# Optimization experiments

Measured on AMD Instinct MI355X. Metric: run time of the kernel, lower is better.

## Reference

```python
import jax, jax.numpy as jnp
import numpy as np

BN_EPS = 1e-5


def setup_inputs() -> dict:
    key = jax.random.key(0)
    ks = jax.random.split(key, 6)
    P, D_IN, H, N_NODES = 2_000_000, 3, 128, 20_000
    x = jax.random.normal(ks[0], (P, D_IN), dtype=jnp.float32)
    batch_idx = jax.random.randint(ks[1], (P,), 0, N_NODES, dtype=jnp.int64)
    W1 = jax.random.normal(ks[2], (D_IN, H), dtype=jnp.float32) * 0.5
    b1 = jax.random.normal(ks[3], (H,), dtype=jnp.float32) * 0.1
    gamma = jnp.ones((H,), dtype=jnp.float32)
    beta = jnp.zeros((H,), dtype=jnp.float32)
    running_mean = jnp.zeros((H,), dtype=jnp.float32)
    running_var = jnp.ones((H,), dtype=jnp.float32)
    W2 = jax.random.normal(ks[4], (H, H), dtype=jnp.float32) * (1.0 / np.sqrt(H))
    b2 = jax.random.normal(ks[5], (H,), dtype=jnp.float32) * 0.1
    return {"x": x, "batch_idx": batch_idx, "num_nodes": N_NODES,
            "W1": W1, "b1": b1, "gamma": gamma, "beta": beta,
            "running_mean": running_mean, "running_var": running_var,
            "W2": W2, "b2": b2}


def reference(x, batch_idx, num_nodes, W1, b1, gamma, beta,
              running_mean, running_var, W2, b2):
    # per-point MLP: Linear -> BatchNorm1d (eval: running stats) -> ReLU -> Linear -> ReLU
    h = x @ W1 + b1                                        # [P, H]
    h = (h - running_mean) * jax.lax.rsqrt(running_var + BN_EPS) * gamma + beta
    h = jax.nn.relu(h)
    h = jax.nn.relu(h @ W2 + b2)                            # [P, H], values >= 0
    # scatter_max by node; torch_scatter fills empty segments with 0,
    # and since h >= 0 post-ReLU, clamping the -inf fill to 0 is exact.
    node_feats = jax.ops.segment_max(h, batch_idx, num_segments=num_nodes)
    return jnp.maximum(node_feats, 0.0)                     # [num_nodes, H]
```

## Files before the change

### kernel.cpp

```cpp
#include <hip/hip_runtime.h>
#include <hip/hip_bf16.h>

#define H 128
#define TILE_PTS 32
#define ROW_STRIDE 136
#define NBLK 512
#define BT 1024
#define BSH 3
#define NPB (1 << BSH)
#define CAP 1024
#define RAWN (CAP + 32)
#define HBUF (TILE_PTS * ROW_STRIDE)

typedef __attribute__((ext_vector_type(8))) short short8;
typedef __attribute__((ext_vector_type(4))) float float4v;
typedef __attribute__((ext_vector_type(2))) float float2v;
typedef __attribute__((ext_vector_type(4))) int int4v;
typedef _Float16 half8 __attribute__((ext_vector_type(8)));
typedef _Float16 half2 __attribute__((ext_vector_type(2)));

static __device__ __forceinline__ unsigned short f2bf(float f) {
    unsigned u = __float_as_uint(f);
    unsigned r = (u + 0x7fffu + ((u >> 16) & 1u)) >> 16;
    return (unsigned short)r;
}
static __device__ __forceinline__ unsigned pkbf(float a, float b) {
    __hip_bfloat162 h = __float22bfloat162_rn(float2{a, b});
    return *reinterpret_cast<unsigned*>(&h);
}
static __device__ __forceinline__ unsigned short f2h(float f) {
    _Float16 h = (_Float16)f;
    unsigned short u;
    __builtin_memcpy(&u, &h, 2);
    return u;
}
static __device__ __forceinline__ float h2f(unsigned short us) {
    _Float16 h;
    __builtin_memcpy(&h, &us, 2);
    return (float)h;
}

__global__ __launch_bounds__(BT)
void scatter_slot(const int* __restrict__ bidx, const float* __restrict__ x,
                  const float* __restrict__ W2, unsigned short* __restrict__ W2T,
                  int* __restrict__ gcnt, uint2* __restrict__ xb,
                  int P, int nbuk) {
    extern __shared__ int lh[];
    const int b = blockIdx.x, t = threadIdx.x;
    for (int i = b * BT + t; i < H * H; i += NBLK * BT) {
        int n = i >> 7, k = i & 127;
        W2T[i] = f2h(W2[k * H + n]);
    }
    for (int i = t; i < nbuk; i += BT) lh[i] = 0;
    __syncthreads();
    const int chunk4 = (((P + NBLK - 1) / NBLK) + 3) & ~3;
    const int lo = b * chunk4;
    const int hi = (lo + chunk4 < P) ? lo + chunk4 : P;
    for (int p4 = lo + 4 * t; p4 < hi; p4 += 4 * BT) {
        if (p4 + 4 <= hi) {
            int4v i4 = *(const int4v*)&bidx[p4];
            atomicAdd(&lh[i4.x >> BSH], 1);
            atomicAdd(&lh[i4.y >> BSH], 1);
            atomicAdd(&lh[i4.z >> BSH], 1);
            atomicAdd(&lh[i4.w >> BSH], 1);
        } else {
            for (int p = p4; p < hi; ++p) atomicAdd(&lh[bidx[p] >> BSH], 1);
        }
    }
    __syncthreads();
    for (int i = t; i < nbuk; i += BT) {
        int c = lh[i];
        lh[i] = (c > 0) ? atomicAdd(&gcnt[i], c) : 0;
    }
    __syncthreads();
    auto emit = [&](int idx, float x0, float x1, float x2) {
        int pos = atomicAdd(&lh[idx >> BSH], 1);
        if (pos < CAP) {
            uint2 r;
            r.x = (unsigned)f2h(x0) | ((unsigned)f2h(x1) << 16);
            r.y = (unsigned)f2h(x2) | ((unsigned)(idx & (NPB - 1)) << 16);
            xb[(size_t)(idx >> BSH) * CAP + pos] = r;
        }
    };
    for (int p4 = lo + 4 * t; p4 < hi; p4 += 4 * BT) {
        if (p4 + 4 <= hi) {
            int4v i4 = *(const int4v*)&bidx[p4];
            float4v xa = *(const float4v*)(x + (size_t)p4 * 3);
            float4v xbv = *(const float4v*)(x + (size_t)p4 * 3 + 4);
            float4v xc = *(const float4v*)(x + (size_t)p4 * 3 + 8);
            emit(i4.x, xa[0], xa[1], xa[2]);
            emit(i4.y, xa[3], xbv[0], xbv[1]);
            emit(i4.z, xbv[2], xbv[3], xc[0]);
            emit(i4.w, xc[1], xc[2], xc[3]);
        } else {
            for (int p = p4; p < hi; ++p)
                emit(bidx[p], x[p * 3 + 0], x[p * 3 + 1], x[p * 3 + 2]);
        }
    }
}

__global__ __launch_bounds__(256, 4)
void node_kernel18(const uint2* __restrict__ xb, const int* __restrict__ gcnt,
                   const float* __restrict__ W1, const float* __restrict__ b1,
                   const float* __restrict__ gamma, const float* __restrict__ beta,
                   const float* __restrict__ rmean, const float* __restrict__ rvar,
                   const unsigned short* __restrict__ W2T, const float* __restrict__ b2,
                   float* __restrict__ out, int N)
{
    __shared__ __align__(16) unsigned short pool[2 * HBUF];
    __shared__ __align__(16) uint2 srt[RAWN];
    __shared__ int basec[NPB + 1];
    __shared__ int curw[4][NPB];

    const int bk   = blockIdx.x;
    const int t    = threadIdx.x;
    const int lane = t & 63;
    const int wave = t >> 6;
    const int g  = t & 15;
    const int q  = t >> 4;
    const int c0 = g * 8;

    half2 w1h[3][4], b1h[4];
    #pragma unroll
    for (int jp = 0; jp < 4; ++jp) {
        #pragma unroll
        for (int e = 0; e < 2; ++e) {
            int c = c0 + 2 * jp + e;
            float sc = gamma[c] * rsqrtf(rvar[c] + 1e-5f);
            w1h[0][jp][e] = (_Float16)(W1[0 * H + c] * sc);
            w1h[1][jp][e] = (_Float16)(W1[1 * H + c] * sc);
            w1h[2][jp][e] = (_Float16)(W1[2 * H + c] * sc);
            b1h[jp][e]    = (_Float16)((b1[c] - rmean[c]) * sc + beta[c]);
        }
    }

    const int bn = lane & 15;
    const int kq = (lane >> 4) * 8;
    half8 bfrag[2][4];
    float  b2v[2];
    #pragma unroll
    for (int nt = 0; nt < 2; ++nt) {
        const int nn = wave * 32 + nt * 16 + bn;
        b2v[nt] = b2[nn];
        #pragma unroll
        for (int kk = 0; kk < 4; ++kk)
            bfrag[nt][kk] = *(const half8*)(const void*)&W2T[nn * H + kk * 32 + kq];
    }

    uint2* raw = (uint2*)pool;
    int n_b = gcnt[bk];
    if (n_b > CAP) n_b = CAP;
    const uint2* src = xb + (size_t)bk * CAP;
    for (int p = t; p < n_b; p += 256) raw[p] = src[p];
    if (t < 4 * NPB) ((int*)curw)[t] = 0;
    __syncthreads();
    for (int p = t; p < n_b; p += 256)
        atomicAdd(&curw[wave][raw[p].y >> 16], 1);
    __syncthreads();
    if (t == 0) {
        int run = 0;
        #pragma unroll
        for (int i = 0; i < NPB; ++i) {
            basec[i] = run;
            #pragma unroll
            for (int w = 0; w < 4; ++w) {
                int c = curw[w][i]; curw[w][i] = run; run += c;
            }
        }
        basec[NPB] = run;
    }
    __syncthreads();
    for (int p = t; p < n_b; p += 256) {
        uint2 r = raw[p];
        int pos = atomicAdd(&curw[wave][r.y >> 16], 1);
        srt[pos] = r;
    }
    for (int p = n_b + t; p < n_b + TILE_PTS; p += 256)
        if (p < RAWN) srt[p] = uint2{0u, 0u};
    __syncthreads();

    const float4v zero4 = {0.f, 0.f, 0.f, 0.f};
    const float NEG_INF = -__builtin_inff();
    const half2 zero2h = {(_Float16)0.f, (_Float16)0.f};
    const int nodebase = bk << BSH;
    const int nlocal = (N - nodebase < NPB) ? (N - nodebase) : NPB;

    const int st0 = q * ROW_STRIDE + c0;
    const int st1 = (q + 16) * ROW_STRIDE + c0;
    const int ar  = bn * ROW_STRIDE + kq;

    #define STAGE_PT(r, hs, so)                                            \
    {                                                                      \
        half2 a0 = __builtin_bit_cast(half2,                               \
            __builtin_amdgcn_perm(0u, (r).x, 0x01000100u));                \
        half2 a1 = __builtin_bit_cast(half2,                               \
            __builtin_amdgcn_perm(0u, (r).x, 0x03020302u));                \
        half2 a2 = __builtin_bit_cast(half2,                               \
            __builtin_amdgcn_perm(0u, (r).y, 0x01000100u));                \
        int4v pk;                                                          \
        _Pragma("unroll")                                                  \
        for (int jp = 0; jp < 4; ++jp) {                                   \
            half2 hh = b1h[jp];                                            \
            hh = __builtin_elementwise_fma(a0, w1h[0][jp], hh);            \
            hh = __builtin_elementwise_fma(a1, w1h[1][jp], hh);            \
            hh = __builtin_elementwise_fma(a2, w1h[2][jp], hh);            \
            hh = __builtin_elementwise_max(hh, zero2h);                    \
            pk[jp] = __builtin_bit_cast(int, hh);                          \
        }                                                                  \
        *(int4v*)(void*)&(hs)[so] = pk;                                    \
    }

    for (int j = 0; j < nlocal; ++j) {
        const int startj = basec[j];
        const int n      = basec[j + 1] - startj;
        const int ntiles = (n + TILE_PTS - 1) >> 5;

        float2v vm0 = {NEG_INF, NEG_INF};
        float2v vm1 = {NEG_INF, NEG_INF};

        if (ntiles > 0) {
            unsigned short* hb = pool;
            unsigned short* hs = pool + HBUF;
            {
                uint2 r0 = srt[startj + q];
                uint2 r1 = srt[startj + q + 16];
                STAGE_PT(r0, hb, st0);
                STAGE_PT(r1, hb, st1);
            }
            __syncthreads();

            for (int tile = 0; tile < ntiles; ++tile) {
                const int tb = tile * TILE_PTS;
                const bool have = (tile + 1 < ntiles);

                uint2 n0, n1;
                if (have) {
                    n0 = srt[startj + tb + TILE_PTS + q];
                    n1 = srt[startj + tb + TILE_PTS + 16 + q];
                }

                float4v acc00, acc01, acc10, acc11;
                {
                    half8 a0v = *(const half8*)(const void*)&hb[ar];
                    half8 a1v = *(const half8*)(const void*)&hb[ar + 16 * ROW_STRIDE];
                    acc00 = __builtin_amdgcn_mfma_f32_16x16x32_f16(a0v, bfrag[0][0], zero4, 0, 0, 0);
                    acc01 = __builtin_amdgcn_mfma_f32_16x16x32_f16(a0v, bfrag[1][0], zero4, 0, 0, 0);
                    acc10 = __builtin_amdgcn_mfma_f32_16x16x32_f16(a1v, bfrag[0][0], zero4, 0, 0, 0);
                    acc11 = __builtin_amdgcn_mfma_f32_16x16x32_f16(a1v, bfrag[1][0], zero4, 0, 0, 0);
                }
                #pragma unroll
                for (int kk = 1; kk < 4; ++kk) {
                    half8 a0v = *(const half8*)(const void*)&hb[ar + kk * 32];
                    half8 a1v = *(const half8*)(const void*)&hb[ar + 16 * ROW_STRIDE + kk * 32];
                    acc00 = __builtin_amdgcn_mfma_f32_16x16x32_f16(a0v, bfrag[0][kk], acc00, 0, 0, 0);
                    acc01 = __builtin_amdgcn_mfma_f32_16x16x32_f16(a0v, bfrag[1][kk], acc01, 0, 0, 0);
                    acc10 = __builtin_amdgcn_mfma_f32_16x16x32_f16(a1v, bfrag[0][kk], acc10, 0, 0, 0);
                    acc11 = __builtin_amdgcn_mfma_f32_16x16x32_f16(a1v, bfrag[1][kk], acc11, 0, 0, 0);
                }

                if (have) {
                    STAGE_PT(n0, hs, st0);
                    STAGE_PT(n1, hs, st1);
                }

                if (tb + TILE_PTS <= n) {
                    vm0 = __builtin_elementwise_max(vm0, float2v{acc00[0], acc00[1]});
                    vm0 = __builtin_elementwise_max(vm0, float2v{acc00[2], acc00[3]});
                    vm0 = __builtin_elementwise_max(vm0, float2v{acc10[0], acc10[1]});
                    vm0 = __builtin_elementwise_max(vm0, float2v{acc10[2], acc10[3]});
                    vm1 = __builtin_elementwise_max(vm1, float2v{acc01[0], acc01[1]});
                    vm1 = __builtin_elementwise_max(vm1, float2v{acc01[2], acc01[3]});
                    vm1 = __builtin_elementwise_max(vm1, float2v{acc11[0], acc11[1]});
                    vm1 = __builtin_elementwise_max(vm1, float2v{acc11[2], acc11[3]});
                } else {
                    const int r0base = (lane >> 4) * 4;
                    #pragma unroll
                    for (int r = 0; r < 4; ++r) {
                        const bool v0 = (tb + r0base + r) < n;
                        const bool v1 = (tb + 16 + r0base + r) < n;
                        vm0[r & 1] = fmaxf(vm0[r & 1], v0 ? acc00[r] : NEG_INF);
                        vm1[r & 1] = fmaxf(vm1[r & 1], v0 ? acc01[r] : NEG_INF);
                        vm0[r & 1] = fmaxf(vm0[r & 1], v1 ? acc10[r] : NEG_INF);
                        vm1[r & 1] = fmaxf(vm1[r & 1], v1 ? acc11[r] : NEG_INF);
                    }
                }
                __syncthreads();
                unsigned short* tmp = hb; hb = hs; hs = tmp;
            }
        }

        float vmax0 = fmaxf(vm0[0], vm0[1]);
        float vmax1 = fmaxf(vm1[0], vm1[1]);
        vmax0 = fmaxf(vmax0, __shfl_xor(vmax0, 16, 64));
        vmax0 = fmaxf(vmax0, __shfl_xor(vmax0, 32, 64));
        vmax1 = fmaxf(vmax1, __shfl_xor(vmax1, 16, 64));
        vmax1 = fmaxf(vmax1, __shfl_xor(vmax1, 32, 64));
        if (lane < 16) {
            float* orow = out + (size_t)(nodebase + j) * H + wave * 32;
            orow[lane]      = fmaxf(vmax0 + b2v[0], 0.f);
            orow[16 + lane] = fmaxf(vmax1 + b2v[1], 0.f);
        }
    }
    #undef STAGE_PT
}

__global__ void histB_kernel(const int* __restrict__ bidx, int* __restrict__ counts, int P) {
    int p = blockIdx.x * 256 + threadIdx.x;
    if (p < P) atomicAdd(&counts[bidx[p]], 1);
}
__global__ __launch_bounds__(1024)
void scanB_kernel(const int* __restrict__ counts, int* __restrict__ starts,
                  int* __restrict__ cursor, int N) {
    __shared__ int sums[1024];
    const int t = threadIdx.x;
    const int chunk = (N + 1023) >> 10;
    const int lo = t * chunk;
    const int hi = (lo + chunk < N) ? lo + chunk : N;
    int s = 0;
    for (int i = lo; i < hi; ++i) s += counts[i];
    sums[t] = s;
    __syncthreads();
    #pragma unroll
    for (int off = 1; off < 1024; off <<= 1) {
        int a = (t >= off) ? sums[t - off] : 0;
        __syncthreads();
        sums[t] += a;
        __syncthreads();
    }
    int run = sums[t] - s;
    for (int i = lo; i < hi; ++i) { starts[i] = run; cursor[i] = run; run += counts[i]; }
    if (t == 1023) starts[N] = sums[1023];
}
__global__ void scatterB_kernel(const int* __restrict__ bidx, const float* __restrict__ x,
                                int* __restrict__ cursor, uint2* __restrict__ xs, int P) {
    int p = blockIdx.x * 256 + threadIdx.x;
    if (p < P) {
        int pos = atomicAdd(&cursor[bidx[p]], 1);
        uint2 r;
        r.x = (unsigned)f2h(x[p * 3 + 0]) | ((unsigned)f2h(x[p * 3 + 1]) << 16);
        r.y = (unsigned)f2h(x[p * 3 + 2]);
        xs[pos] = r;
    }
}
__global__ void convw2_kernel(const float* __restrict__ W2, unsigned short* __restrict__ W2T) {
    int i = blockIdx.x * 256 + threadIdx.x;
    if (i < H * H) {
        int n = i >> 7, k = i & 127;
        W2T[i] = f2bf(W2[k * H + n]);
    }
}

__global__ __launch_bounds__(256, 4)
void node_kernelB(const uint2* __restrict__ xs,
                  const int*   __restrict__ starts,
                  const float* __restrict__ W1, const float* __restrict__ b1,
                  const float* __restrict__ gamma, const float* __restrict__ beta,
                  const float* __restrict__ rmean, const float* __restrict__ rvar,
                  const unsigned short* __restrict__ W2T, const float* __restrict__ b2,
                  float* __restrict__ out, int N)
{
    __shared__ __align__(16) unsigned short h1s[2][TILE_PTS * ROW_STRIDE];
    const int t = threadIdx.x, lane = t & 63, wave = t >> 6;
    const int g = t & 15, q = t >> 4, c0 = g * 8;
    float2v w1f2[3][4], b1f2[4];
    #pragma unroll
    for (int jp = 0; jp < 4; ++jp)
        #pragma unroll
        for (int e = 0; e < 2; ++e) {
            int c = c0 + 2 * jp + e;
            float sc = gamma[c] * rsqrtf(rvar[c] + 1e-5f);
            w1f2[0][jp][e] = W1[0 * H + c] * sc;
            w1f2[1][jp][e] = W1[1 * H + c] * sc;
            w1f2[2][jp][e] = W1[2 * H + c] * sc;
            b1f2[jp][e]    = (b1[c] - rmean[c]) * sc + beta[c];
        }
    const int bn = lane & 15, kq = (lane >> 4) * 8;
    short8 bfrag[2][4]; float b2v[2];
    #pragma unroll
    for (int nt = 0; nt < 2; ++nt) {
        const int nn = wave * 32 + nt * 16 + bn;
        b2v[nt] = b2[nn];
        #pragma unroll
        for (int kk = 0; kk < 4; ++kk)
            bfrag[nt][kk] = *(const short8*)&W2T[nn * H + kk * 32 + kq];
    }
    const float4v zero4 = {0.f, 0.f, 0.f, 0.f};
    const float NEG_INF = -__builtin_inff();
    const float2v zero2 = {0.f, 0.f};
    for (int node = blockIdx.x; node < N; node += gridDim.x) {
        const int start = starts[node];
        const int n = starts[node + 1] - start;
        const int ntiles = (n + TILE_PTS - 1) >> 5;
        float2v vmax2[2];
        vmax2[0] = float2v{NEG_INF, NEG_INF};
        vmax2[1] = float2v{NEG_INF, NEG_INF};
        auto loadx = [&](int tb, float xv[2][3]) {
            #pragma unroll
            for (int i = 0; i < 2; ++i) {
                uint2 r = xs[start + tb + q + 16 * i];
                xv[i][0] = h2f((unsigned short)(r.x & 0xffffu));
                xv[i][1] = h2f((unsigned short)(r.x >> 16));
                xv[i][2] = h2f((unsigned short)(r.y & 0xffffu));
            }
        };
        auto stage = [&](const float xv[2][3], unsigned short* buf) {
            #pragma unroll
            for (int i = 0; i < 2; ++i) {
                const int pl = q + 16 * i;
                float2v a0 = {xv[i][0], xv[i][0]};
                float2v a1 = {xv[i][1], xv[i][1]};
                float2v a2 = {xv[i][2], xv[i][2]};
                int4v pk;
                #pragma unroll
                for (int jp = 0; jp < 4; ++jp) {
                    float2v h = b1f2[jp];
                    h = __builtin_elementwise_fma(a0, w1f2[0][jp], h);
                    h = __builtin_elementwise_fma(a1, w1f2[1][jp], h);
                    h = __builtin_elementwise_fma(a2, w1f2[2][jp], h);
                    h = __builtin_elementwise_max(h, zero2);
                    pk[jp] = (int)pkbf(h[0], h[1]);
                }
                *(int4v*)(void*)&buf[pl * ROW_STRIDE + c0] = pk;
            }
        };
        if (ntiles > 0) {
            float xv[2][3];
            loadx(0, xv);
            stage(xv, h1s[0]);
            __syncthreads();
            int pb = 0;
            for (int tile = 0; tile < ntiles; ++tile) {
                const int tb = tile * TILE_PTS;
                const bool havenext = (tile + 1 < ntiles);
                float nx[2][3];
                if (havenext) loadx(tb + TILE_PTS, nx);
                float4v acc[2][2];
                const unsigned short* hb = h1s[pb];
                {
                    short8 a0 = *(const short8*)&hb[bn * ROW_STRIDE + kq];
                    short8 a1 = *(const short8*)&hb[(16 + bn) * ROW_STRIDE + kq];
                    #pragma unroll
                    for (int nt = 0; nt < 2; ++nt) {
                        acc[0][nt] = __builtin_amdgcn_mfma_f32_16x16x32_bf16(a0, bfrag[nt][0], zero4, 0, 0, 0);
                        acc[1][nt] = __builtin_amdgcn_mfma_f32_16x16x32_bf16(a1, bfrag[nt][0], zero4, 0, 0, 0);
                    }
                }
                #pragma unroll
                for (int kk = 1; kk < 4; ++kk) {
                    short8 a0 = *(const short8*)&hb[bn * ROW_STRIDE + kk * 32 + kq];
                    short8 a1 = *(const short8*)&hb[(16 + bn) * ROW_STRIDE + kk * 32 + kq];
                    #pragma unroll
                    for (int nt = 0; nt < 2; ++nt) {
                        acc[0][nt] = __builtin_amdgcn_mfma_f32_16x16x32_bf16(a0, bfrag[nt][kk], acc[0][nt], 0, 0, 0);
                        acc[1][nt] = __builtin_amdgcn_mfma_f32_16x16x32_bf16(a1, bfrag[nt][kk], acc[1][nt], 0, 0, 0);
                    }
                }
                if (havenext) stage(nx, h1s[pb ^ 1]);
                if (tb + TILE_PTS <= n) {
                    #pragma unroll
                    for (int ps = 0; ps < 2; ++ps)
                        #pragma unroll
                        for (int nt = 0; nt < 2; ++nt) {
                            vmax2[nt] = __builtin_elementwise_max(vmax2[nt],
                                          float2v{acc[ps][nt][0], acc[ps][nt][1]});
                            vmax2[nt] = __builtin_elementwise_max(vmax2[nt],
                                          float2v{acc[ps][nt][2], acc[ps][nt][3]});
                        }
                } else {
                    #pragma unroll
                    for (int ps = 0; ps < 2; ++ps)
                        #pragma unroll
                        for (int r = 0; r < 4; ++r) {
                            const int pl = ps * 16 + (lane >> 4) * 4 + r;
                            const bool valid = (tb + pl) < n;
                            vmax2[0][r & 1] = fmaxf(vmax2[0][r & 1], valid ? acc[ps][0][r] : NEG_INF);
                            vmax2[1][r & 1] = fmaxf(vmax2[1][r & 1], valid ? acc[ps][1][r] : NEG_INF);
                        }
                }
                __syncthreads();
                pb ^= 1;
            }
        }
        float vmax0 = fmaxf(vmax2[0][0], vmax2[0][1]);
        float vmax1 = fmaxf(vmax2[1][0], vmax2[1][1]);
        vmax0 = fmaxf(vmax0, __shfl_xor(vmax0, 16, 64));
        vmax0 = fmaxf(vmax0, __shfl_xor(vmax0, 32, 64));
        vmax1 = fmaxf(vmax1, __shfl_xor(vmax1, 16, 64));
        vmax1 = fmaxf(vmax1, __shfl_xor(vmax1, 32, 64));
        if (lane < 16) {
            float* orow = out + (size_t)node * H + wave * 32;
            orow[lane]      = fmaxf(vmax0 + b2v[0], 0.f);
            orow[16 + lane] = fmaxf(vmax1 + b2v[1], 0.f);
        }
    }
}

extern "C" void kernel_launch(void* const* d_in, const int* in_sizes, int n_in,
                              void* d_out, int out_size, void* d_ws, size_t ws_size,
                              hipStream_t stream) {
    const float* x     = (const float*)d_in[0];
    const int*   bidx  = (const int*)  d_in[1];
    const float* W1    = (const float*)d_in[3];
    const float* b1    = (const float*)d_in[4];
    const float* gamma = (const float*)d_in[5];
    const float* beta  = (const float*)d_in[6];
    const float* rmean = (const float*)d_in[7];
    const float* rvar  = (const float*)d_in[8];
    const float* W2    = (const float*)d_in[9];
    const float* b2    = (const float*)d_in[10];
    float* out = (float*)d_out;

    const int P = in_sizes[1];
    const int N = out_size / H;
    const int nbuk = (N + NPB - 1) >> BSH;

    const size_t szW2T = 32768;
    const size_t szG   = (size_t)4 * ((nbuk + 63) & ~63);
    const size_t szXb  = (size_t)8 * ((size_t)CAP * nbuk + 64);
    const size_t needA = szW2T + szG + szXb + 256;
    const size_t lds1  = (size_t)4 * nbuk;

    char* w = (char*)d_ws;

    if (lds1 <= 60000 && ws_size >= needA) {
        unsigned short* W2T = (unsigned short*)w;
        int* gcnt = (int*)(w + szW2T);
        uint2* xb = (uint2*)(w + szW2T + szG);

        hipMemsetAsync(gcnt, 0, (size_t)nbuk * sizeof(int), stream);
        scatter_slot<<<NBLK, BT, lds1, stream>>>(bidx, x, W2, W2T, gcnt, xb, P, nbuk);
        node_kernel18<<<nbuk, 256, 0, stream>>>(xb, gcnt, W1, b1, gamma, beta,
                                                rmean, rvar, W2T, b2, out, N);
        return;
    }

    const int Npad = (N + 63) & ~63;
    const size_t szStarts = (size_t)4 * (Npad + 64);
    const size_t szCnt    = (size_t)4 * Npad;
    const size_t szRec    = (size_t)8 * (P + 64);
    const size_t needB    = szStarts + szW2T + 2 * szCnt + szRec + 256;
    if (ws_size >= needB) {
        int* starts = (int*)w;
        unsigned short* W2T = (unsigned short*)(w + szStarts);
        int* counts = (int*)(w + szStarts + szW2T);
        int* cursor = (int*)(w + szStarts + szW2T + szCnt);
        uint2* xs   = (uint2*)(w + szStarts + szW2T + 2 * szCnt);

        hipMemsetAsync(counts, 0, (size_t)N * sizeof(int), stream);
        const int pblocks = (P + 255) / 256;
        const int grid = (N < 2048) ? N : 2048;
        convw2_kernel<<<(H * H + 255) / 256, 256, 0, stream>>>(W2, W2T);
        histB_kernel<<<pblocks, 256, 0, stream>>>(bidx, counts, P);
        scanB_kernel<<<1, 1024, 0, stream>>>(counts, starts, cursor, N);
        scatterB_kernel<<<pblocks, 256, 0, stream>>>(bidx, x, cursor, xs, P);
        node_kernelB<<<grid, 256, 0, stream>>>(xs, starts, W1, b1, gamma, beta,
                                               rmean, rvar, W2T, b2, out, N);
    }
}
```

Baseline: 218.6 us.

## Replace two-pass LDS histogram scatter with one-pass partitioned global-atomic bucketing

Removes the per-block LDS histogram, prefix and reservation passes of the scatter kernel. Each point now takes a slot with a global atomic on a per-bucket counter that is split into 8 partitions, chosen by block index, and each partition has a capacity of 160. The node kernel gathers the partitions back into its local buffer. This cuts one full read of batch_idx and the block synchronisations, and spreads atomic contention across partitions. In exchange it adds up to 2M global atomics and risks dropping points when a single partition overflows its capacity of 160, which is tighter than the old per-bucket cap of 1024.

```diff
diff --git a/kernel.cpp b/kernel.cpp
--- a/kernel.cpp
+++ b/kernel.cpp
@@ -4,8 +4,8 @@
 #define H 128
 #define TILE_PTS 32
 #define ROW_STRIDE 136
-#define NBLK 512
-#define BT 1024
+#define NBLK1 2048
+#define BT1 256
 #define BSH 3
 #define NPB (1 << BSH)
 #define CAP 1024
@@ -40,72 +40,52 @@
     return (float)h;
 }
 
-__global__ __launch_bounds__(BT)
-void scatter_slot(const int* __restrict__ bidx, const float* __restrict__ x,
-                  const float* __restrict__ W2, unsigned short* __restrict__ W2T,
-                  int* __restrict__ gcnt, uint2* __restrict__ xb,
-                  int P, int nbuk) {
-    extern __shared__ int lh[];
+__global__ __launch_bounds__(BT1)
+void scatter_onepass(const int* __restrict__ bidx, const float* __restrict__ x,
+                     const float* __restrict__ W2, unsigned short* __restrict__ W2T,
+                     int* __restrict__ gcnt, uint2* __restrict__ xb,
+                     int P, int nparts, int capp) {
     const int b = blockIdx.x, t = threadIdx.x;
-    for (int i = b * BT + t; i < H * H; i += NBLK * BT) {
+    const int gt = b * BT1 + t;
+    const int part = b & (nparts - 1);
+    for (int i = gt; i < H * H; i += NBLK1 * BT1) {
         int n = i >> 7, k = i & 127;
         W2T[i] = f2h(W2[k * H + n]);
     }
-    for (int i = t; i < nbuk; i += BT) lh[i] = 0;
-    __syncthreads();
-    const int chunk4 = (((P + NBLK - 1) / NBLK) + 3) & ~3;
-    const int lo = b * chunk4;
-    const int hi = (lo + chunk4 < P) ? lo + chunk4 : P;
-    for (int p4 = lo + 4 * t; p4 < hi; p4 += 4 * BT) {
-        if (p4 + 4 <= hi) {
-            int4v i4 = *(const int4v*)&bidx[p4];
-            atomicAdd(&lh[i4.x >> BSH], 1);
-            atomicAdd(&lh[i4.y >> BSH], 1);
-            atomicAdd(&lh[i4.z >> BSH], 1);
-            atomicAdd(&lh[i4.w >> BSH], 1);
-        } else {
-            for (int p = p4; p < hi; ++p) atomicAdd(&lh[bidx[p] >> BSH], 1);
-        }
-    }
-    __syncthreads();
-    for (int i = t; i < nbuk; i += BT) {
-        int c = lh[i];
-        lh[i] = (c > 0) ? atomicAdd(&gcnt[i], c) : 0;
-    }
-    __syncthreads();
     auto emit = [&](int idx, float x0, float x1, float x2) {
-        int pos = atomicAdd(&lh[idx >> BSH], 1);
-        if (pos < CAP) {
+        int pos = atomicAdd(&gcnt[(idx >> BSH) * nparts + part], 1);
+        if (pos < capp) {
             uint2 r;
             r.x = (unsigned)f2h(x0) | ((unsigned)f2h(x1) << 16);
             r.y = (unsigned)f2h(x2) | ((unsigned)(idx & (NPB - 1)) << 16);
-            xb[(size_t)(idx >> BSH) * CAP + pos] = r;
+            xb[((size_t)(idx >> BSH) * nparts + part) * capp + pos] = r;
         }
     };
-    for (int p4 = lo + 4 * t; p4 < hi; p4 += 4 * BT) {
-        if (p4 + 4 <= hi) {
+    const int stride4 = NBLK1 * BT1 * 4;
+    for (int p4 = gt * 4; p4 < P; p4 += stride4) {
+        if (p4 + 4 <= P) {
             int4v i4 = *(const int4v*)&bidx[p4];
-            float4v xa = *(const float4v*)(x + (size_t)p4 * 3);
+            float4v xa  = *(const float4v*)(x + (size_t)p4 * 3);
             float4v xbv = *(const float4v*)(x + (size_t)p4 * 3 + 4);
-            float4v xc = *(const float4v*)(x + (size_t)p4 * 3 + 8);
+            float4v xc  = *(const float4v*)(x + (size_t)p4 * 3 + 8);
             emit(i4.x, xa[0], xa[1], xa[2]);
             emit(i4.y, xa[3], xbv[0], xbv[1]);
             emit(i4.z, xbv[2], xbv[3], xc[0]);
             emit(i4.w, xc[1], xc[2], xc[3]);
         } else {
-            for (int p = p4; p < hi; ++p)
+            for (int p = p4; p < P; ++p)
                 emit(bidx[p], x[p * 3 + 0], x[p * 3 + 1], x[p * 3 + 2]);
         }
     }
 }
 
 __global__ __launch_bounds__(256, 4)
-void node_kernel18(const uint2* __restrict__ xb, const int* __restrict__ gcnt,
+void node_kernel19(const uint2* __restrict__ xb, const int* __restrict__ gcnt,
                    const float* __restrict__ W1, const float* __restrict__ b1,
                    const float* __restrict__ gamma, const float* __restrict__ beta,
                    const float* __restrict__ rmean, const float* __restrict__ rvar,
                    const unsigned short* __restrict__ W2T, const float* __restrict__ b2,
-                   float* __restrict__ out, int N)
+                   float* __restrict__ out, int N, int nparts, int capp)
 {
     __shared__ __align__(16) unsigned short pool[2 * HBUF];
     __shared__ __align__(16) uint2 srt[RAWN];
@@ -148,10 +128,15 @@
     }
 
     uint2* raw = (uint2*)pool;
-    int n_b = gcnt[bk];
-    if (n_b > CAP) n_b = CAP;
-    const uint2* src = xb + (size_t)bk * CAP;
-    for (int p = t; p < n_b; p += 256) raw[p] = src[p];
+    int n_b = 0;
+    for (int p = 0; p < nparts; ++p) {
+        int cp = gcnt[bk * nparts + p];
+        if (cp > capp) cp = capp;
+        int take = (cp < CAP - n_b) ? cp : (CAP - n_b);
+        const uint2* srcp = xb + ((size_t)bk * nparts + p) * capp;
+        for (int i = t; i < take; i += 256) raw[n_b + i] = srcp[i];
+        n_b += take;
+    }
     if (t < 4 * NPB) ((int*)curw)[t] = 0;
     __syncthreads();
     for (int p = t; p < n_b; p += 256)
@@ -513,25 +498,44 @@
     const int P = in_sizes[1];
     const int N = out_size / H;
     const int nbuk = (N + NPB - 1) >> BSH;
-
     const size_t szW2T = 32768;
-    const size_t szG   = (size_t)4 * ((nbuk + 63) & ~63);
-    const size_t szXb  = (size_t)8 * ((size_t)CAP * nbuk + 64);
-    const size_t needA = szW2T + szG + szXb + 256;
-    const size_t lds1  = (size_t)4 * nbuk;
-
     char* w = (char*)d_ws;
 
-    if (lds1 <= 60000 && ws_size >= needA) {
-        unsigned short* W2T = (unsigned short*)w;
-        int* gcnt = (int*)(w + szW2T);
-        uint2* xb = (uint2*)(w + szW2T + szG);
-
-        hipMemsetAsync(gcnt, 0, (size_t)nbuk * sizeof(int), stream);
-        scatter_slot<<<NBLK, BT, lds1, stream>>>(bidx, x, W2, W2T, gcnt, xb, P, nbuk);
-        node_kernel18<<<nbuk, 256, 0, stream>>>(xb, gcnt, W1, b1, gamma, beta,
-                                                rmean, rvar, W2T, b2, out, N);
-        return;
+    {
+        const int npa = 8, cpa = 160;
+        const size_t szG  = (size_t)4 * (((size_t)nbuk * npa + 63) & ~(size_t)63);
+        const size_t szXb = (size_t)8 * ((size_t)cpa * npa * nbuk + 64);
+        const size_t need = szW2T + szG + szXb + 256;
+        if (ws_size >= need) {
+            unsigned short* W2T = (unsigned short*)w;
+            int* gcnt = (int*)(w + szW2T);
+            uint2* xb = (uint2*)(w + szW2T + szG);
+            hipMemsetAsync(gcnt, 0, (size_t)nbuk * npa * sizeof(int), stream);
+            scatter_onepass<<<NBLK1, BT1, 0, stream>>>(bidx, x, W2, W2T, gcnt, xb,
+                                                       P, npa, cpa);
+            node_kernel19<<<nbuk, 256, 0, stream>>>(xb, gcnt, W1, b1, gamma, beta,
+                                                    rmean, rvar, W2T, b2, out, N,
+                                                    npa, cpa);
+            return;
+        }
+    }
+    {
+        const int npa = 1, cpa = CAP;
+        const size_t szG  = (size_t)4 * (((size_t)nbuk + 63) & ~(size_t)63);
+        const size_t szXb = (size_t)8 * ((size_t)cpa * nbuk + 64);
+        const size_t need = szW2T + szG + szXb + 256;
+        if (ws_size >= need) {
+            unsigned short* W2T = (unsigned short*)w;
+            int* gcnt = (int*)(w + szW2T);
+            uint2* xb = (uint2*)(w + szW2T + szG);
+            hipMemsetAsync(gcnt, 0, (size_t)nbuk * sizeof(int), stream);
+            scatter_onepass<<<NBLK1, BT1, 0, stream>>>(bidx, x, W2, W2T, gcnt, xb,
+                                                       P, npa, cpa);
+            node_kernel19<<<nbuk, 256, 0, stream>>>(xb, gcnt, W1, b1, gamma, beta,
+                                                    rmean, rvar, W2T, b2, out, N,
+                                                    npa, cpa);
+            return;
+        }
     }
 
     const int Npad = (N + 63) & ~63;
```

Result: slower. 277.9 us (+27.1%).

## Replace global atomic bucket reservation with per-block histogram, scan, and scatter

Applied to the files above, without the earlier changes.

The single scatter kernel used global atomics per block per bucket to reserve output slots. It is now split into three kernels: a per-block histogram written to a counts matrix, a column-wise prefix scan that yields deterministic per-block offsets and bucket totals, and a scatter pass that re-reads the inputs. The block count also drops from 512 to 256. This removes global atomic contention and the memset, but adds two extra launches, a second full pass over bidx, and a 256×nbuk counts/offsets matrix in global memory.

```diff
diff --git a/kernel.cpp b/kernel.cpp
--- a/kernel.cpp
+++ b/kernel.cpp
@@ -4,8 +4,8 @@
 #define H 128
 #define TILE_PTS 32
 #define ROW_STRIDE 136
-#define NBLK 512
-#define BT 1024
+#define NBLKH 256
+#define BTH 1024
 #define BSH 3
 #define NPB (1 << BSH)
 #define CAP 1024
@@ -40,23 +40,22 @@
     return (float)h;
 }
 
-__global__ __launch_bounds__(BT)
-void scatter_slot(const int* __restrict__ bidx, const float* __restrict__ x,
-                  const float* __restrict__ W2, unsigned short* __restrict__ W2T,
-                  int* __restrict__ gcnt, uint2* __restrict__ xb,
-                  int P, int nbuk) {
+__global__ __launch_bounds__(BTH)
+void hist_kernel(const int* __restrict__ bidx,
+                 const float* __restrict__ W2, unsigned short* __restrict__ W2T,
+                 int* __restrict__ counts, int P, int nbuk, int nbukP) {
     extern __shared__ int lh[];
     const int b = blockIdx.x, t = threadIdx.x;
-    for (int i = b * BT + t; i < H * H; i += NBLK * BT) {
+    for (int i = b * BTH + t; i < H * H; i += NBLKH * BTH) {
         int n = i >> 7, k = i & 127;
         W2T[i] = f2h(W2[k * H + n]);
     }
-    for (int i = t; i < nbuk; i += BT) lh[i] = 0;
-    __syncthreads();
-    const int chunk4 = (((P + NBLK - 1) / NBLK) + 3) & ~3;
+    for (int i = t; i < nbuk; i += BTH) lh[i] = 0;
+    __syncthreads();
+    const int chunk4 = (((P + NBLKH - 1) / NBLKH) + 3) & ~3;
     const int lo = b * chunk4;
     const int hi = (lo + chunk4 < P) ? lo + chunk4 : P;
-    for (int p4 = lo + 4 * t; p4 < hi; p4 += 4 * BT) {
+    for (int p4 = lo + 4 * t; p4 < hi; p4 += 4 * BTH) {
         if (p4 + 4 <= hi) {
             int4v i4 = *(const int4v*)&bidx[p4];
             atomicAdd(&lh[i4.x >> BSH], 1);
@@ -68,13 +67,40 @@
         }
     }
     __syncthreads();
-    for (int i = t; i < nbuk; i += BT) {
-        int c = lh[i];
-        lh[i] = (c > 0) ? atomicAdd(&gcnt[i], c) : 0;
-    }
+    int* row = counts + (size_t)b * nbukP;
+    for (int i = t; i < nbuk; i += BTH) row[i] = lh[i];
+}
+
+__global__ __launch_bounds__(NBLKH)
+void scan_kernel(const int* __restrict__ counts, int* __restrict__ offs,
+                 int* __restrict__ total, int nbukP) {
+    __shared__ int s[NBLKH];
+    const int bk = blockIdx.x, t = threadIdx.x;
+    const int c = counts[(size_t)t * nbukP + bk];
+    s[t] = c;
+    __syncthreads();
+    #pragma unroll
+    for (int off = 1; off < NBLKH; off <<= 1) {
+        int a = (t >= off) ? s[t - off] : 0;
+        __syncthreads();
+        s[t] += a;
+        __syncthreads();
+    }
+    offs[(size_t)t * nbukP + bk] = s[t] - c;
+    if (t == NBLKH - 1) total[bk] = s[t];
+}
+
+__global__ __launch_bounds__(BTH)
+void scatter_kernel(const int* __restrict__ bidx, const float* __restrict__ x,
+                    const int* __restrict__ offs, uint2* __restrict__ xb,
+                    int P, int nbuk, int nbukP) {
+    extern __shared__ int cur[];
+    const int b = blockIdx.x, t = threadIdx.x;
+    const int* row = offs + (size_t)b * nbukP;
+    for (int i = t; i < nbuk; i += BTH) cur[i] = row[i];
     __syncthreads();
     auto emit = [&](int idx, float x0, float x1, float x2) {
-        int pos = atomicAdd(&lh[idx >> BSH], 1);
+        int pos = atomicAdd(&cur[idx >> BSH], 1);
         if (pos < CAP) {
             uint2 r;
             r.x = (unsigned)f2h(x0) | ((unsigned)f2h(x1) << 16);
@@ -82,12 +108,15 @@
             xb[(size_t)(idx >> BSH) * CAP + pos] = r;
         }
     };
-    for (int p4 = lo + 4 * t; p4 < hi; p4 += 4 * BT) {
+    const int chunk4 = (((P + NBLKH - 1) / NBLKH) + 3) & ~3;
+    const int lo = b * chunk4;
+    const int hi = (lo + chunk4 < P) ? lo + chunk4 : P;
+    for (int p4 = lo + 4 * t; p4 < hi; p4 += 4 * BTH) {
         if (p4 + 4 <= hi) {
             int4v i4 = *(const int4v*)&bidx[p4];
-            float4v xa = *(const float4v*)(x + (size_t)p4 * 3);
+            float4v xa  = *(const float4v*)(x + (size_t)p4 * 3);
             float4v xbv = *(const float4v*)(x + (size_t)p4 * 3 + 4);
-            float4v xc = *(const float4v*)(x + (size_t)p4 * 3 + 8);
+            float4v xc  = *(const float4v*)(x + (size_t)p4 * 3 + 8);
             emit(i4.x, xa[0], xa[1], xa[2]);
             emit(i4.y, xa[3], xbv[0], xbv[1]);
             emit(i4.z, xbv[2], xbv[3], xc[0]);
@@ -100,7 +129,7 @@
 }
 
 __global__ __launch_bounds__(256, 4)
-void node_kernel18(const uint2* __restrict__ xb, const int* __restrict__ gcnt,
+void node_kernel20(const uint2* __restrict__ xb, const int* __restrict__ total,
                    const float* __restrict__ W1, const float* __restrict__ b1,
                    const float* __restrict__ gamma, const float* __restrict__ beta,
                    const float* __restrict__ rmean, const float* __restrict__ rvar,
@@ -148,7 +177,7 @@
     }
 
     uint2* raw = (uint2*)pool;
-    int n_b = gcnt[bk];
+    int n_b = total[bk];
     if (n_b > CAP) n_b = CAP;
     const uint2* src = xb + (size_t)bk * CAP;
     for (int p = t; p < n_b; p += 256) raw[p] = src[p];
@@ -513,25 +542,33 @@
     const int P = in_sizes[1];
     const int N = out_size / H;
     const int nbuk = (N + NPB - 1) >> BSH;
-
+    const int nbukP = (nbuk + 63) & ~63;
     const size_t szW2T = 32768;
-    const size_t szG   = (size_t)4 * ((nbuk + 63) & ~63);
-    const size_t szXb  = (size_t)8 * ((size_t)CAP * nbuk + 64);
-    const size_t needA = szW2T + szG + szXb + 256;
     const size_t lds1  = (size_t)4 * nbuk;
-
     char* w = (char*)d_ws;
 
-    if (lds1 <= 60000 && ws_size >= needA) {
-        unsigned short* W2T = (unsigned short*)w;
-        int* gcnt = (int*)(w + szW2T);
-        uint2* xb = (uint2*)(w + szW2T + szG);
-
-        hipMemsetAsync(gcnt, 0, (size_t)nbuk * sizeof(int), stream);
-        scatter_slot<<<NBLK, BT, lds1, stream>>>(bidx, x, W2, W2T, gcnt, xb, P, nbuk);
-        node_kernel18<<<nbuk, 256, 0, stream>>>(xb, gcnt, W1, b1, gamma, beta,
-                                                rmean, rvar, W2T, b2, out, N);
-        return;
+    {
+        const size_t szTot = (size_t)4 * nbukP;
+        const size_t szCnt = (size_t)4 * NBLKH * nbukP;
+        const size_t szOff = szCnt;
+        const size_t szXb  = (size_t)8 * ((size_t)CAP * nbuk + 64);
+        const size_t need  = szW2T + szTot + szCnt + szOff + szXb + 256;
+        if (lds1 <= 60000 && ws_size >= need) {
+            unsigned short* W2T = (unsigned short*)w;
+            int* total  = (int*)(w + szW2T);
+            int* counts = (int*)(w + szW2T + szTot);
+            int* offs   = (int*)(w + szW2T + szTot + szCnt);
+            uint2* xb   = (uint2*)(w + szW2T + szTot + szCnt + szOff);
+
+            hist_kernel<<<NBLKH, BTH, lds1, stream>>>(bidx, W2, W2T, counts,
+                                                      P, nbuk, nbukP);
+            scan_kernel<<<nbuk, NBLKH, 0, stream>>>(counts, offs, total, nbukP);
+            scatter_kernel<<<NBLKH, BTH, lds1, stream>>>(bidx, x, offs, xb,
+                                                         P, nbuk, nbukP);
+            node_kernel20<<<nbuk, 256, 0, stream>>>(xb, total, W1, b1, gamma, beta,
+                                                    rmean, rvar, W2T, b2, out, N);
+            return;
+        }
     }
 
     const int Npad = (N + 63) & ~63;
```

Result: no change. 220.1 us (+0.7%).

## Split point binning into two-level superbucket then fine scatter passes

Applied to the files above, without the earlier changes.

Replaces the single-pass scatter into 2500 eight-node buckets with a coarse pass into 256-node superbuckets, followed by a second kernel that splits each superbucket into fine buckets across two half-partitions. The node kernel now gathers points from multiple partitions per bucket. The intent is to cut the scattered, poorly coalesced global writes and LDS atomic contention of the fine-grained scatter, since coarse buckets give denser write streams. In exchange it adds an extra kernel launch and a full extra read/write round trip of the packed point records, and the fixed capacities (SBCAP, CAPP) can drop points if a bucket overflows.

```diff
diff --git a/kernel.cpp b/kernel.cpp
--- a/kernel.cpp
+++ b/kernel.cpp
@@ -4,13 +4,18 @@
 #define H 128
 #define TILE_PTS 32
 #define ROW_STRIDE 136
-#define NBLK 512
-#define BT 1024
+#define NBLKA 256
+#define BTA 1024
 #define BSH 3
 #define NPB (1 << BSH)
-#define CAP 1024
+#define CAP 1088
 #define RAWN (CAP + 32)
 #define HBUF (TILE_PTS * ROW_STRIDE)
+
+#define SBF 32
+#define SBNODES (SBF * NPB)
+#define SBCAP 26624
+#define CAPP 544
 
 typedef __attribute__((ext_vector_type(8))) short short8;
 typedef __attribute__((ext_vector_type(4))) float float4v;
@@ -40,23 +45,118 @@
     return (float)h;
 }
 
-__global__ __launch_bounds__(BT)
+__global__ __launch_bounds__(BTA)
+void scatter_sb(const int* __restrict__ bidx, const float* __restrict__ x,
+                const float* __restrict__ W2, unsigned short* __restrict__ W2T,
+                int* __restrict__ sbcnt, uint2* __restrict__ sbx,
+                int P, int nsb) {
+    extern __shared__ int lh[];
+    const int b = blockIdx.x, t = threadIdx.x;
+    for (int i = b * BTA + t; i < H * H; i += NBLKA * BTA) {
+        int n = i >> 7, k = i & 127;
+        W2T[i] = f2h(W2[k * H + n]);
+    }
+    for (int i = t; i < nsb; i += BTA) lh[i] = 0;
+    __syncthreads();
+    const int chunk4 = (((P + NBLKA - 1) / NBLKA) + 3) & ~3;
+    const int lo = b * chunk4;
+    const int hi = (lo + chunk4 < P) ? lo + chunk4 : P;
+    for (int p4 = lo + 4 * t; p4 < hi; p4 += 4 * BTA) {
+        if (p4 + 4 <= hi) {
+            int4v i4 = *(const int4v*)&bidx[p4];
+            atomicAdd(&lh[i4.x / SBNODES], 1);
+            atomicAdd(&lh[i4.y / SBNODES], 1);
+            atomicAdd(&lh[i4.z / SBNODES], 1);
+            atomicAdd(&lh[i4.w / SBNODES], 1);
+        } else {
+            for (int p = p4; p < hi; ++p) atomicAdd(&lh[bidx[p] / SBNODES], 1);
+        }
+    }
+    __syncthreads();
+    for (int i = t; i < nsb; i += BTA) {
+        int c = lh[i];
+        lh[i] = (c > 0) ? atomicAdd(&sbcnt[i], c) : 0;
+    }
+    __syncthreads();
+    auto emit = [&](int idx, float x0, float x1, float x2) {
+        int sb = idx / SBNODES;
+        int pos = atomicAdd(&lh[sb], 1);
+        if (pos < SBCAP) {
+            uint2 r;
+            r.x = (unsigned)f2h(x0) | ((unsigned)f2h(x1) << 16);
+            r.y = (unsigned)f2h(x2) | ((unsigned)(idx & (SBNODES - 1)) << 16);
+            sbx[(size_t)sb * SBCAP + pos] = r;
+        }
+    };
+    for (int p4 = lo + 4 * t; p4 < hi; p4 += 4 * BTA) {
+        if (p4 + 4 <= hi) {
+            int4v i4 = *(const int4v*)&bidx[p4];
+            float4v xa  = *(const float4v*)(x + (size_t)p4 * 3);
+            float4v xbv = *(const float4v*)(x + (size_t)p4 * 3 + 4);
+            float4v xc  = *(const float4v*)(x + (size_t)p4 * 3 + 8);
+            emit(i4.x, xa[0], xa[1], xa[2]);
+            emit(i4.y, xa[3], xbv[0], xbv[1]);
+            emit(i4.z, xbv[2], xbv[3], xc[0]);
+            emit(i4.w, xc[1], xc[2], xc[3]);
+        } else {
+            for (int p = p4; p < hi; ++p)
+                emit(bidx[p], x[p * 3 + 0], x[p * 3 + 1], x[p * 3 + 2]);
+        }
+    }
+}
+
+__global__ __launch_bounds__(BTA)
+void scatter_fine(const uint2* __restrict__ sbx, const int* __restrict__ sbcnt,
+                  uint2* __restrict__ xb, int* __restrict__ gcnt2,
+                  int nbuk, int nsb) {
+    __shared__ int cur[SBF];
+    const int sb   = blockIdx.x >> 1;
+    const int half = blockIdx.x & 1;
+    const int t    = threadIdx.x;
+    if (t < SBF) cur[t] = 0;
+    __syncthreads();
+    int cnt = sbcnt[sb];
+    if (cnt > SBCAP) cnt = SBCAP;
+    const int start = half ? (cnt >> 1) : 0;
+    const int end   = half ? cnt : (cnt >> 1);
+    const uint2* src = sbx + (size_t)sb * SBCAP;
+    for (int p = start + t; p < end; p += BTA) {
+        uint2 r = src[p];
+        const int fb  = (r.y >> (16 + BSH)) & (SBF - 1);
+        const int buk = sb * SBF + fb;
+        int pos = atomicAdd(&cur[fb], 1);
+        if (buk < nbuk && pos < CAPP) {
+            r.y &= 0x0007FFFFu;
+            xb[((size_t)buk * 2 + half) * CAPP + pos] = r;
+        }
+    }
+    __syncthreads();
+    if (t < SBF) {
+        const int buk = sb * SBF + t;
+        if (buk < nbuk) {
+            int c = cur[t];
+            gcnt2[buk * 2 + half] = (c < CAPP) ? c : CAPP;
+        }
+    }
+}
+
+__global__ __launch_bounds__(BTA)
 void scatter_slot(const int* __restrict__ bidx, const float* __restrict__ x,
                   const float* __restrict__ W2, unsigned short* __restrict__ W2T,
                   int* __restrict__ gcnt, uint2* __restrict__ xb,
-                  int P, int nbuk) {
+                  int P, int nbuk, int cap1) {
     extern __shared__ int lh[];
     const int b = blockIdx.x, t = threadIdx.x;
-    for (int i = b * BT + t; i < H * H; i += NBLK * BT) {
+    for (int i = b * BTA + t; i < H * H; i += NBLKA * BTA) {
         int n = i >> 7, k = i & 127;
         W2T[i] = f2h(W2[k * H + n]);
     }
-    for (int i = t; i < nbuk; i += BT) lh[i] = 0;
-    __syncthreads();
-    const int chunk4 = (((P + NBLK - 1) / NBLK) + 3) & ~3;
+    for (int i = t; i < nbuk; i += BTA) lh[i] = 0;
+    __syncthreads();
+    const int chunk4 = (((P + NBLKA - 1) / NBLKA) + 3) & ~3;
     const int lo = b * chunk4;
     const int hi = (lo + chunk4 < P) ? lo + chunk4 : P;
-    for (int p4 = lo + 4 * t; p4 < hi; p4 += 4 * BT) {
+    for (int p4 = lo + 4 * t; p4 < hi; p4 += 4 * BTA) {
         if (p4 + 4 <= hi) {
             int4v i4 = *(const int4v*)&bidx[p4];
             atomicAdd(&lh[i4.x >> BSH], 1);
@@ -68,26 +168,26 @@
         }
     }
     __syncthreads();
-    for (int i = t; i < nbuk; i += BT) {
+    for (int i = t; i < nbuk; i += BTA) {
         int c = lh[i];
         lh[i] = (c > 0) ? atomicAdd(&gcnt[i], c) : 0;
     }
     __syncthreads();
     auto emit = [&](int idx, float x0, float x1, float x2) {
         int pos = atomicAdd(&lh[idx >> BSH], 1);
-        if (pos < CAP) {
+        if (pos < cap1) {
             uint2 r;
             r.x = (unsigned)f2h(x0) | ((unsigned)f2h(x1) << 16);
             r.y = (unsigned)f2h(x2) | ((unsigned)(idx & (NPB - 1)) << 16);
-            xb[(size_t)(idx >> BSH) * CAP + pos] = r;
+            xb[(size_t)(idx >> BSH) * cap1 + pos] = r;
         }
     };
-    for (int p4 = lo + 4 * t; p4 < hi; p4 += 4 * BT) {
+    for (int p4 = lo + 4 * t; p4 < hi; p4 += 4 * BTA) {
         if (p4 + 4 <= hi) {
             int4v i4 = *(const int4v*)&bidx[p4];
-            float4v xa = *(const float4v*)(x + (size_t)p4 * 3);
+            float4v xa  = *(const float4v*)(x + (size_t)p4 * 3);
             float4v xbv = *(const float4v*)(x + (size_t)p4 * 3 + 4);
-            float4v xc = *(const float4v*)(x + (size_t)p4 * 3 + 8);
+            float4v xc  = *(const float4v*)(x + (size_t)p4 * 3 + 8);
             emit(i4.x, xa[0], xa[1], xa[2]);
             emit(i4.y, xa[3], xbv[0], xbv[1]);
             emit(i4.z, xbv[2], xbv[3], xc[0]);
@@ -100,12 +200,12 @@
 }
 
 __global__ __launch_bounds__(256, 4)
-void node_kernel18(const uint2* __restrict__ xb, const int* __restrict__ gcnt,
+void node_kernel22(const uint2* __restrict__ xb, const int* __restrict__ gcnt,
                    const float* __restrict__ W1, const float* __restrict__ b1,
                    const float* __restrict__ gamma, const float* __restrict__ beta,
                    const float* __restrict__ rmean, const float* __restrict__ rvar,
                    const unsigned short* __restrict__ W2T, const float* __restrict__ b2,
-                   float* __restrict__ out, int N)
+                   float* __restrict__ out, int N, int nparts, int capp)
 {
     __shared__ __align__(16) unsigned short pool[2 * HBUF];
     __shared__ __align__(16) uint2 srt[RAWN];
@@ -148,14 +248,19 @@
     }
 
     uint2* raw = (uint2*)pool;
-    int n_b = gcnt[bk];
-    if (n_b > CAP) n_b = CAP;
-    const uint2* src = xb + (size_t)bk * CAP;
-    for (int p = t; p < n_b; p += 256) raw[p] = src[p];
+    int n_b = 0;
+    for (int p = 0; p < nparts; ++p) {
+        int cp = gcnt[bk * nparts + p];
+        if (cp > capp) cp = capp;
+        int take = (cp < CAP - n_b) ? cp : (CAP - n_b);
+        const uint2* srcp = xb + ((size_t)bk * nparts + p) * capp;
+        for (int i = t; i < take; i += 256) raw[n_b + i] = srcp[i];
+        n_b += take;
+    }
     if (t < 4 * NPB) ((int*)curw)[t] = 0;
     __syncthreads();
     for (int p = t; p < n_b; p += 256)
-        atomicAdd(&curw[wave][raw[p].y >> 16], 1);
+        atomicAdd(&curw[wave][(raw[p].y >> 16) & (NPB - 1)], 1);
     __syncthreads();
     if (t == 0) {
         int run = 0;
@@ -172,7 +277,7 @@
     __syncthreads();
     for (int p = t; p < n_b; p += 256) {
         uint2 r = raw[p];
-        int pos = atomicAdd(&curw[wave][r.y >> 16], 1);
+        int pos = atomicAdd(&curw[wave][(r.y >> 16) & (NPB - 1)], 1);
         srt[pos] = r;
     }
     for (int p = n_b + t; p < n_b + TILE_PTS; p += 256)
@@ -513,25 +618,54 @@
     const int P = in_sizes[1];
     const int N = out_size / H;
     const int nbuk = (N + NPB - 1) >> BSH;
-
+    const int nsb  = (N + SBNODES - 1) / SBNODES;
     const size_t szW2T = 32768;
-    const size_t szG   = (size_t)4 * ((nbuk + 63) & ~63);
-    const size_t szXb  = (size_t)8 * ((size_t)CAP * nbuk + 64);
-    const size_t needA = szW2T + szG + szXb + 256;
-    const size_t lds1  = (size_t)4 * nbuk;
-
     char* w = (char*)d_ws;
 
-    if (lds1 <= 60000 && ws_size >= needA) {
-        unsigned short* W2T = (unsigned short*)w;
-        int* gcnt = (int*)(w + szW2T);
-        uint2* xb = (uint2*)(w + szW2T + szG);
-
-        hipMemsetAsync(gcnt, 0, (size_t)nbuk * sizeof(int), stream);
-        scatter_slot<<<NBLK, BT, lds1, stream>>>(bidx, x, W2, W2T, gcnt, xb, P, nbuk);
-        node_kernel18<<<nbuk, 256, 0, stream>>>(xb, gcnt, W1, b1, gamma, beta,
-                                                rmean, rvar, W2T, b2, out, N);
-        return;
+    {
+        const size_t szSbc = (size_t)4 * ((nsb + 127) & ~127);
+        const size_t szG2  = (size_t)4 * (((size_t)nbuk * 2 + 63) & ~(size_t)63);
+        const size_t szSbx = (size_t)8 * ((size_t)SBCAP * nsb + 64);
+        const size_t szXb  = (size_t)8 * ((size_t)CAPP * 2 * nbuk + 64);
+        const size_t need  = szW2T + szSbc + szG2 + szSbx + szXb + 256;
+        const size_t ldsA  = (size_t)4 * nsb;
+        if (ws_size >= need && ldsA <= 60000) {
+            unsigned short* W2T = (unsigned short*)w;
+            int* sbcnt = (int*)(w + szW2T);
+            int* gcnt2 = (int*)(w + szW2T + szSbc);
+            uint2* sbx = (uint2*)(w + szW2T + szSbc + szG2);
+            uint2* xb  = (uint2*)(w + szW2T + szSbc + szG2 + szSbx);
+
+            hipMemsetAsync(sbcnt, 0, szSbc, stream);
+            scatter_sb<<<NBLKA, BTA, ldsA, stream>>>(bidx, x, W2, W2T, sbcnt, sbx,
+                                                     P, nsb);
+            scatter_fine<<<nsb * 2, BTA, 0, stream>>>(sbx, sbcnt, xb, gcnt2,
+                                                      nbuk, nsb);
+            node_kernel22<<<nbuk, 256, 0, stream>>>(xb, gcnt2, W1, b1, gamma, beta,
+                                                    rmean, rvar, W2T, b2, out, N,
+                                                    2, CAPP);
+            return;
+        }
+    }
+
+    {
+        const int cap1 = 1024;
+        const size_t szG  = (size_t)4 * (((size_t)nbuk + 63) & ~(size_t)63);
+        const size_t szXb = (size_t)8 * ((size_t)cap1 * nbuk + 64);
+        const size_t need = szW2T + szG + szXb + 256;
+        const size_t lds1 = (size_t)4 * nbuk;
+        if (ws_size >= need && lds1 <= 60000) {
+            unsigned short* W2T = (unsigned short*)w;
+            int* gcnt = (int*)(w + szW2T);
+            uint2* xb = (uint2*)(w + szW2T + szG);
+            hipMemsetAsync(gcnt, 0, (size_t)nbuk * sizeof(int), stream);
+            scatter_slot<<<NBLKA, BTA, lds1, stream>>>(bidx, x, W2, W2T, gcnt, xb,
+                                                       P, nbuk, cap1);
+            node_kernel22<<<nbuk, 256, 0, stream>>>(xb, gcnt, W1, b1, gamma, beta,
+                                                    rmean, rvar, W2T, b2, out, N,
+                                                    1, cap1);
+            return;
+        }
     }
 
     const int Npad = (N + 63) & ~63;
```

Result: faster. 209.3 us, median of 2 (-4.3%).
